# Kernel optimization log

Hardware: AMD Instinct MI355X
Metric: run time of the kernel (lower is better)

## Reference

```python
import jax, jax.numpy as jnp
import numpy as np

B_IN = 30    # input sphere bandwidth
B_MID = 16   # bandwidth after S2 conv
B_OUT = 10   # bandwidth after SO3 conv
F0, F1 = 100, 100
NUM_CLS = 40
EPS = 1e-5


def _wigner_d(l, betas):
    """Real Wigner-d matrices d^l_{mn}(beta) -> [len(betas), 2l+1, 2l+1] (numpy)."""
    betas = np.asarray(betas, np.float64)
    n = 2 * l + 1
    if l == 0:
        return np.ones((betas.size, 1, 1))
    m = np.arange(-l, l)
    c = np.sqrt(l * (l + 1) - m * (m + 1))      # <m+1|J+|m>
    Jp = np.zeros((n, n)); Jp[np.arange(1, n), np.arange(n - 1)] = c
    K = -(Jp - Jp.T) / 2.0                      # K = -i*Jy, real antisymmetric; d = exp(beta*K)
    w, V = np.linalg.eigh(1j * K)
    ph = np.exp(-1j * np.outer(betas, w))
    return np.einsum('ij,bj,kj->bik', V, ph, V.conj()).real


def _dh(b):
    """Driscoll-Healy beta samples and quadrature weights for bandwidth b."""
    k = np.arange(2 * b)
    beta = np.pi * (2 * k + 1) / (4 * b)
    j = np.arange(b)
    w = (2.0 / b) * np.sin(beta) * (np.sin(np.outer(2 * k + 1, 2 * j + 1) * np.pi / (4 * b)) @ (1.0 / (2 * j + 1)))
    return beta, w


def _project(x, b):
    """Point cloud [B,3,N] -> radial distance image on S2 grid [B,1,2b,2b] (beta, alpha)."""
    nb = 2 * b
    r = jnp.linalg.norm(x, axis=1)                                   # [B,N]
    beta = jnp.arccos(jnp.clip(x[:, 2] / jnp.maximum(r, 1e-8), -1.0, 1.0))
    alpha = jnp.mod(jnp.arctan2(x[:, 1], x[:, 0]), 2.0 * np.pi)
    bi = jnp.clip((beta / np.pi * nb).astype(jnp.int32), 0, nb - 1)
    ai = jnp.clip((alpha / (2.0 * np.pi) * nb).astype(jnp.int32), 0, nb - 1)
    Bb = x.shape[0]
    flat = (jnp.arange(Bb)[:, None] * nb * nb + bi * nb + ai).reshape(-1)
    img = jnp.zeros((Bb * nb * nb,), x.dtype).at[flat].max(r.reshape(-1))
    return img.reshape(Bb, 1, nb, nb)


def _s2_fft(x, b_out):
    """x [B,C,2b,2b] (beta,alpha) -> list over l of fhat^l_m [B,C,2l+1] complex."""
    N = x.shape[-1]
    beta, qw = _dh(N // 2)
    G = jnp.fft.fft(x.astype(jnp.complex64), axis=-1)                # coeff of e^{-im alpha}
    out = []
    for l in range(b_out):
        d0 = _wigner_d(l, beta)[:, :, l]                             # d^l_{m,0}(beta_k)
        wd = jnp.asarray(qw[:, None] * d0 * (2 * np.pi / N), jnp.complex64)
        mi = np.arange(-l, l + 1) % N
        out.append(jnp.einsum('km,bckm->bcm', wd, G[..., mi]))
    return out


def _s2_rft(w, b_out, n_alpha):
    """Dirac kernel on equatorial S2 grid (beta=pi/2) -> list over l of [f_in,f_out,2l+1]."""
    alphas = 2 * np.pi * np.arange(n_alpha) / n_alpha
    wc = w.astype(jnp.complex64) / n_alpha
    out = []
    for l in range(b_out):
        m = np.arange(-l, l + 1)
        basis = _wigner_d(l, [np.pi / 2])[0][:, l][:, None] * np.exp(-1j * np.outer(m, alphas))
        out.append(jnp.einsum('mp,iop->iom', jnp.asarray(basis, jnp.complex64), wc))
    return out


def _so3_fft(x, b_out):
    """x [B,C,2b,2b,2b] (beta,alpha,gamma) -> list over l of [B,C,2l+1,2l+1]."""
    N = x.shape[-1]
    beta, qw = _dh(N // 2)
    G = jnp.fft.fft2(x.astype(jnp.complex64), axes=(-2, -1))
    out = []
    for l in range(b_out):
        d = _wigner_d(l, beta)
        wd = jnp.asarray(qw[:, None, None] * d * (2 * np.pi / N) ** 2, jnp.complex64)
        mi = np.arange(-l, l + 1) % N
        out.append(jnp.einsum('kmn,bckmn->bcmn', wd, G[..., mi[:, None], mi[None, :]]))
    return out


def _so3_rft(w, b_out, n_alpha):
    """Dirac kernel on equatorial SO3 grid (beta=pi/2, gamma=0) -> list of [f_in,f_out,2l+1,2l+1]."""
    alphas = 2 * np.pi * np.arange(n_alpha) / n_alpha
    wc = w.astype(jnp.complex64) / n_alpha
    out = []
    for l in range(b_out):
        m = np.arange(-l, l + 1)
        d = _wigner_d(l, [np.pi / 2])[0]
        basis = d[None] * np.exp(-1j * np.outer(alphas, m))[:, :, None]   # [P,2l+1,2l+1]
        out.append(jnp.einsum('pmn,iop->iomn', jnp.asarray(basis, jnp.complex64), wc))
    return out


def _so3_ifft(Z, b_out):
    """Spectral blocks (list over l of [B,f,2l+1,2l+1]) -> x [B,f,2b,2b,2b] real."""
    N = 2 * b_out
    beta, _ = _dh(b_out)
    Bb, f = Z[0].shape[:2]
    M = jnp.zeros((Bb, f, N, N, N), jnp.complex64)
    for l, Zl in enumerate(Z):
        d = jnp.asarray((2 * l + 1) * _wigner_d(l, beta), jnp.complex64)
        mi = np.arange(-l, l + 1) % N
        M = M.at[:, :, :, mi[:, None], mi[None, :]].add(jnp.einsum('kmn,bfmn->bfkmn', d, Zl))
    return (jnp.fft.ifft2(M, axes=(-2, -1)) * (N * N)).real


def _bn_relu(x, g, b):
    mu = x.mean(axis=(0, 2, 3, 4), keepdims=True)
    var = ((x - mu) ** 2).mean(axis=(0, 2, 3, 4), keepdims=True)
    y = (x - mu) * jax.lax.rsqrt(var + EPS) * g[None, :, None, None, None] + b[None, :, None, None, None]
    return jax.nn.relu(y)


def _so3_integrate(x):
    b = x.shape[-1] // 2
    _, qw = _dh(b)
    return jnp.einsum('bfkag,k->bf', x, jnp.asarray(qw, x.dtype)) * (2 * np.pi / (2 * b)) ** 2


def _forward(x, w_s2, bias_s2, bn1_g, bn1_b, w_so3, bias_so3, bn2_g, bn2_b, lin_w, lin_b):
    img = _project(x, B_IN)                                   # [B,1,60,60]
    X = _s2_fft(img, B_MID)
    Y = _s2_rft(w_s2, B_MID, 2 * B_IN)
    # correlation theorem on S2: Z^l_{mn} = sum_i X^l_{i,m} conj(Y^l_{i,n})
    Z = [jnp.einsum('bim,ion->bomn', Xl, jnp.conj(Yl)) for Xl, Yl in zip(X, Y)]
    h = _so3_ifft(Z, B_MID) + bias_s2[None, :, None, None, None]   # [B,100,32,32,32]
    h = _bn_relu(h, bn1_g, bn1_b)
    X2 = _so3_fft(h, B_OUT)
    Y2 = _so3_rft(w_so3, B_OUT, 2 * B_MID)
    # correlation theorem on SO3: Z^l = X^l @ Y^l^dagger (feature-contracted)
    Z2 = [jnp.einsum('bimk,ionk->bomn', Xl, jnp.conj(Yl)) for Xl, Yl in zip(X2, Y2)]
    h2 = _so3_ifft(Z2, B_OUT) + bias_so3[None, :, None, None, None]  # [B,100,20,20,20]
    h2 = _bn_relu(h2, bn2_g, bn2_b)
    feat = _so3_integrate(h2)                                 # [B,100]
    return feat @ lin_w + lin_b                               # cls_logits [B,40]


def setup_inputs() -> dict:
    key = jax.random.key(0)
    ks = jax.random.split(key, 4)
    B, Np = 8, 1024
    return {
        'x': jax.random.normal(ks[0], (B, 3, Np), jnp.float32),
        'w_s2': jax.random.normal(ks[1], (1, F0, 2 * B_IN), jnp.float32) * 0.1,
        'bias_s2': jnp.zeros((F0,), jnp.float32),
        'bn1_g': jnp.ones((F0,), jnp.float32),
        'bn1_b': jnp.zeros((F0,), jnp.float32),
        'w_so3': jax.random.normal(ks[2], (F0, F1, 2 * B_MID), jnp.float32) * 0.1,
        'bias_so3': jnp.zeros((F1,), jnp.float32),
        'bn2_g': jnp.ones((F1,), jnp.float32),
        'bn2_b': jnp.zeros((F1,), jnp.float32),
        'lin_w': jax.random.normal(ks[3], (F1, NUM_CLS), jnp.float32) * 0.1,
        'lin_b': jnp.zeros((NUM_CLS,), jnp.float32),
    }


def reference(x, w_s2, bias_s2, bn1_g, bn1_b, w_so3, bias_so3, bn2_g, bn2_b, lin_w, lin_b):
    return _forward(x, w_s2, bias_s2, bn1_g, bn1_b, w_so3, bias_so3, bn2_g, bn2_b, lin_w, lin_b)
```

## Files before the change

### kernel.cpp

```cpp
#include <hip/hip_runtime.h>
#include <math.h>

#ifndef M_PI
#define M_PI 3.14159265358979323846
#endif

#define TBL_MAGIC 0x5EED5EEDCAFEF00EULL

__device__ const int c_off2[11] = {0,1,10,35,84,165,286,455,680,969,1330};
__device__ const int c_offH[11] = {0,1,7,22,50,95,161,252,372,525,715};
__device__ const int c_T[17] = {0,1,3,6,10,15,21,28,36,45,55,66,78,91,105,120,136};

__device__ constexpr float CS32[32] = {
  1.0f, 0.98078528f, 0.92387953f, 0.83146961f, 0.70710678f, 0.55557023f, 0.38268343f, 0.19509032f,
  0.0f,-0.19509032f,-0.38268343f,-0.55557023f,-0.70710678f,-0.83146961f,-0.92387953f,-0.98078528f,
 -1.0f,-0.98078528f,-0.92387953f,-0.83146961f,-0.70710678f,-0.55557023f,-0.38268343f,-0.19509032f,
  0.0f, 0.19509032f, 0.38268343f, 0.55557023f, 0.70710678f, 0.83146961f, 0.92387953f, 0.98078528f};
__device__ constexpr float SN32[32] = {
  0.0f, 0.19509032f, 0.38268343f, 0.55557023f, 0.70710678f, 0.83146961f, 0.92387953f, 0.98078528f,
  1.0f, 0.98078528f, 0.92387953f, 0.83146961f, 0.70710678f, 0.55557023f, 0.38268343f, 0.19509032f,
  0.0f,-0.19509032f,-0.38268343f,-0.55557023f,-0.70710678f,-0.83146961f,-0.92387953f,-0.98078528f,
 -1.0f,-0.98078528f,-0.92387953f,-0.83146961f,-0.70710678f,-0.55557023f,-0.38268343f,-0.19509032f};

__device__ __forceinline__ int l_from_sq(int off){ int l=0; while((l+1)*(l+1)<=off) l++; return l; }
__device__ __forceinline__ int l_from_offH(int off){ int l=0; while(c_offH[l+1]<=off) l++; return l; }
__device__ __forceinline__ int l_from_T(int c){ int l=0; while(c_T[l+1]<=c) l++; return l; }

__global__ void k_delta(double* Dd, float* Df, const unsigned long long* __restrict__ tflag){
  if (tflag[0]==TBL_MAGIC) return;
  int l = blockIdx.x; int n = 2*l+1; int n2=n*n;
  __shared__ double A[961], T[961], Tm[961];
  for (int idx=threadIdx.x; idx<n2; idx+=1024){
    int r=idx/n, c=idx-r*n;
    double v=0.0;
    if (r==c+1){ double m=(double)(c-l); v = -0.5*sqrt((double)l*(l+1)-m*(m+1)); }
    else if (c==r+1){ double m=(double)(r-l); v = 0.5*sqrt((double)l*(l+1)-m*(m+1)); }
    A[idx] = v*(M_PI*0.5/128.0);
    T[idx] = (r==c)?1.0:0.0;
  }
  __syncthreads();
  for (int j=14; j>=1; --j){
    for (int idx=threadIdx.x; idx<n2; idx+=1024){
      int r=idx/n, c=idx-r*n; double acc=0.0;
      if (r>0)   acc += A[r*n+(r-1)]*T[(r-1)*n+c];
      if (r<n-1) acc += A[r*n+(r+1)]*T[(r+1)*n+c];
      Tm[idx]=acc;
    }
    __syncthreads();
    for (int idx=threadIdx.x; idx<n2; idx+=1024){
      int r=idx/n, c=idx-r*n;
      T[idx] = ((r==c)?1.0:0.0) + Tm[idx]/(double)j;
    }
    __syncthreads();
  }
  for (int s=0; s<7; ++s){
    for (int idx=threadIdx.x; idx<n2; idx+=1024){
      int r=idx/n, c=idx-r*n; double acc=0.0;
      for (int q=0;q<n;q++) acc += T[r*n+q]*T[q*n+c];
      Tm[idx]=acc;
    }
    __syncthreads();
    for (int idx=threadIdx.x; idx<n2; idx+=1024) T[idx]=Tm[idx];
    __syncthreads();
  }
  for (int idx=threadIdx.x; idx<n2; idx+=1024){ Dd[l*961+idx]=T[idx]; Df[l*961+idx]=(float)T[idx]; }
}

__global__ void k_qw(float* qw30, float* qw16, float* qw10, float2* ph32, float2* ph20, float2* ph60,
                     const unsigned long long* __restrict__ tflag){
  if (tflag[0]==TBL_MAGIC) return;
  int t=threadIdx.x;
  if (t<60){
    double beta=M_PI*(2*t+1)/120.0, s=0.0;
    for (int j=0;j<30;j++) s += sin((double)(2*t+1)*(2*j+1)*M_PI/120.0)/(double)(2*j+1);
    qw30[t]=(float)((2.0/30.0)*sin(beta)*s);
    double a=2.0*M_PI*t/60.0; ph60[t]=make_float2((float)cos(a),(float)sin(a));
  }
  if (t<32){
    double beta=M_PI*(2*t+1)/64.0, s=0.0;
    for (int j=0;j<16;j++) s += sin((double)(2*t+1)*(2*j+1)*M_PI/64.0)/(double)(2*j+1);
    qw16[t]=(float)((2.0/16.0)*sin(beta)*s);
    double a=2.0*M_PI*t/32.0; ph32[t]=make_float2((float)cos(a),(float)sin(a));
  }
  if (t<20){
    double beta=M_PI*(2*t+1)/40.0, s=0.0;
    for (int j=0;j<10;j++) s += sin((double)(2*t+1)*(2*j+1)*M_PI/40.0)/(double)(2*j+1);
    qw10[t]=(float)((2.0/10.0)*sin(beta)*s);
    double a=2.0*M_PI*t/20.0; ph20[t]=make_float2((float)cos(a),(float)sin(a));
  }
}

__global__ void k_tables(const double* Dd, const float* qw30, const float* qw16, const float* qw10,
                         float* wd_s2, float* dif16, float* wd16, float* dif10t,
                         const unsigned long long* __restrict__ tflag){
  if (tflag[0]==TBL_MAGIC) return;
  int bid=blockIdx.x;
  __shared__ double cc[32], ss[32];
  int l,k,mode; double beta;
  if (bid<960){ mode=0; l=bid/60; k=bid%60; beta=M_PI*(2*k+1)/120.0; }
  else if (bid<1472){ mode=1; int q=bid-960; l=q/32; k=q%32; beta=M_PI*(2*k+1)/64.0; }
  else { mode=2; int q=bid-1472; l=q/20; k=q%20; beta=M_PI*(2*k+1)/40.0; }
  int n=2*l+1;
  for (int kk=threadIdx.x; kk<=l; kk+=256){ cc[kk]=cos(kk*beta); ss[kk]=sin(kk*beta); }
  __syncthreads();
  const double* D = Dd + l*961;
  if (mode==0){
    for (int mm=threadIdx.x; mm<n; mm+=256){
      int m=mm-l; int p=((m)%4+4)%4; double s=0.0;
      for (int kk=-l; kk<=l; ++kk){
        int ak = kk<0?-kk:kk;
        double c=cc[ak], sn=(kk<0)?-ss[ak]:ss[ak];
        double f=(p==0)?c:(p==1)?sn:(p==2)?-c:-sn;
        s += D[(kk+l)*n+mm]*D[(kk+l)*n+l]*f;
      }
      wd_s2[(l*60+k)*31+mm] = (float)(s*(double)qw30[k]*(2.0*M_PI/60.0));
    }
  } else if (mode==1){
    for (int idx=threadIdx.x; idx<n*n; idx+=256){
      int mm=idx/n, nn=idx-mm*n; int m=mm-l, nb=nn-l;
      int p=((m-nb)%4+4)%4; double s=0.0;
      for (int kk=-l; kk<=l; ++kk){
        int ak = kk<0?-kk:kk;
        double c=cc[ak], sn=(kk<0)?-ss[ak]:ss[ak];
        double f=(p==0)?c:(p==1)?sn:(p==2)?-c:-sn;
        s += D[(kk+l)*n+mm]*D[(kk+l)*n+nn]*f;
      }
      dif16[(size_t)(l*32+k)*961+idx] = (float)((2*l+1)*s);
      if (l<10) wd16[(size_t)(l*32+k)*361+idx] = (float)(s*(double)qw16[k]*(2.0*M_PI/32.0)*(2.0*M_PI/32.0));
    }
  } else {
    for (int idx=threadIdx.x; idx<n*n; idx+=256){
      int mm=idx/n, nn=idx-mm*n; int m=mm-l, nb=nn-l;
      int p=((m-nb)%4+4)%4; double s=0.0;
      for (int kk=-l; kk<=l; ++kk){
        int ak = kk<0?-kk:kk;
        double c=cc[ak], sn=(kk<0)?-ss[ak]:ss[ak];
        double f=(p==0)?c:(p==1)?sn:(p==2)?-c:-sn;
        s += D[(kk+l)*n+mm]*D[(kk+l)*n+nn]*f;
      }
      if (mm>=l){
        int ms=mm-l, n9=nn-l+9;
        dif10t[((size_t)k*10+l)*190 + ms*19 + n9] = (float)((2*l+1)*s);
      }
    }
  }
}

__global__ void k_prep(unsigned long long* tflag, float* img, double2* part){
  int gid = blockIdx.x*256 + threadIdx.x;
  if (gid==0) tflag[0]=TBL_MAGIC;
  for (int i=gid; i<28800; i+=8192) img[i]=0.f;
  for (int i=gid; i<800;   i+=8192) part[i]=make_double2(0.0,0.0);
}

__global__ void k_project(const float* x, float* img){
  int tid = blockIdx.x*256+threadIdx.x;
  if (tid>=8192) return;
  int b=tid>>10, n=tid&1023;
  float px=x[(b*3+0)*1024+n], py=x[(b*3+1)*1024+n], pz=x[(b*3+2)*1024+n];
  float r = sqrtf(px*px+py*py+pz*pz);
  float rc = fmaxf(r, 1e-8f);
  float ct = fminf(1.f, fmaxf(-1.f, pz/rc));
  float beta = acosf(ct);
  float alpha = atan2f(py, px);
  const float TWO_PI = 6.283185307179586f;
  alpha = fmodf(alpha, TWO_PI); if (alpha<0.f) alpha += TWO_PI;
  int bi = (int)(beta/3.14159265358979323846f*60.f); bi = min(59, max(0, bi));
  int ai = (int)(alpha/TWO_PI*60.f);                 ai = min(59, max(0, ai));
  atomicMax((int*)&img[(b*60+bi)*60+ai], __float_as_int(r));
}

__global__ __launch_bounds__(256) void k_front(const float* __restrict__ img, const float2* __restrict__ ph60,
                                               const float* __restrict__ wd_s2, float2* __restrict__ X,
                                               const float* __restrict__ w_s2, const float* __restrict__ Df,
                                               float2* __restrict__ YC,
                                               const float* __restrict__ w_so3, const float2* __restrict__ ph32g,
                                               float2* __restrict__ WH2){
  int bid=blockIdx.x; int t=threadIdx.x;
  if (bid<8){
    int b=bid;
    __shared__ float im[3600];
    __shared__ float2 G[960];
    __shared__ float2 ph[60];
    if (t<60) ph[t]=ph60[t];
    for (int i=t;i<3600;i+=256) im[i]=img[b*3600+i];
    __syncthreads();
    for (int i=t;i<960;i+=256){
      int k=i>>4, m=i&15;
      float sr=0.f, si=0.f;
      const float* imk=&im[k*60];
      for (int a=0;a<60;a++){ float v=imk[a]; float2 p=ph[(m*a)%60]; sr+=v*p.x; si-=v*p.y; }
      G[(k<<4)+m]=make_float2(sr,si);
    }
    __syncthreads();
    int off=t;
    int l=0; while((l+1)*(l+1)<=off) l++;
    int mm=off-l*l; int m=mm-l; int am = m<0?-m:m;
    float xr=0.f, xi=0.f;
    for (int k=0;k<60;k++){
      float w=wd_s2[(l*60+k)*31+mm];
      float2 g=G[(k<<4)+am];
      float gi = (m<0)? -g.y : g.y;
      xr += w*g.x; xi += w*gi;
    }
    X[b*256+off]=make_float2(xr,xi);
  } else if (bid<108){
    int f=bid-8;
    __shared__ float wv[60];
    __shared__ float2 W[16];
    for (int p=t;p<60;p+=256) wv[p]=w_s2[f*60+p];
    __syncthreads();
    if (t<16){
      float sr=0.f, si=0.f;
      for (int p=0;p<60;p++){ float2 p2=ph60[(t*p)%60]; sr+=wv[p]*p2.x; si-=wv[p]*p2.y; }
      W[t]=make_float2(sr/60.f, si/60.f);
    }
    __syncthreads();
    {
      int off=t;
      int l=0; while((l+1)*(l+1)<=off) l++;
      int mm=off-l*l; int m=mm-l; int am=m<0?-m:m;
      float dh=Df[l*961 + mm*(2*l+1) + l];
      float2 wm=W[am];
      float wi = (m>=0)? -wm.y : wm.y;
      YC[f*256+off]=make_float2(dh*wm.x, dh*wi);
    }
  } else {
    int tid=(bid-108)*256+t;
    if (tid<10000){
      int i=tid/100, o=tid-i*100;
      float wv2[32];
      for (int p=0;p<32;p++) wv2[p]=w_so3[(i*100+o)*32+p];
      for (int m=0;m<10;m++){
        float sr=0.f, si=0.f;
        for (int p=0;p<32;p++){ float2 p2=ph32g[(m*p)&31]; sr+=wv2[p]*p2.x; si-=wv2[p]*p2.y; }
        WH2[((size_t)m*100+i)*100+o]=make_float2(sr/32.f, si/32.f);
      }
    }
  }
}

__global__ void k_u(const float2* X, const float* dif16, const float2* ph32g, float2* u){
  int bid=blockIdx.x;
  int l, k, ns0, ns1;
  if (bid < 256){ l = bid>>5; k = bid&31; ns0=0; ns1=l+1; }
  else {
    int q=bid-256; l = 8 + (q>>6); int half=(q>>5)&1; k=q&31;
    int mid=(l+2)>>1;
    ns0 = half? mid : 0; ns1 = half? (l+1) : mid;
  }
  int n=2*l+1;
  __shared__ float d[961];
  __shared__ float2 Xs[8][31];
  __shared__ float2 ph[32];
  int t=threadIdx.x;
  if (t<32) ph[t]=ph32g[t];
  for (int i=t;i<n*n;i+=256) d[i]=dif16[(size_t)(l*32+k)*961+i];
  if (t<8*n){ int b=t/n, mm=t-b*n; Xs[b][mm]=X[b*256+l*l+mm]; }
  __syncthreads();
  int b=t>>5, a=t&31;
  float2* up = u + (size_t)(b*32+k)*4488 + a;
  for (int ns=ns0; ns<ns1; ++ns){
    float ar=0.f, ai=0.f;
    int nn = ns + l;
    for (int mm=0; mm<n; ++mm){
      float2 x=Xs[b][mm];
      float2 p=ph[((mm-l)*a)&31];
      float pr=x.x*p.x-x.y*p.y, pi=x.x*p.y+x.y*p.x;
      float dv=d[mm*n+nn];
      ar += dv*pr; ai += dv*pi;
    }
    up[(size_t)(c_T[l]+ns)*33]=make_float2(ar,ai);
  }
}

#define KH_F 8
__global__ __launch_bounds__(512,4) void k_h(const float2* __restrict__ u, const float2* __restrict__ YC,
                                             float* __restrict__ h, double2* __restrict__ part){
  int bid=blockIdx.x;
  int fg = bid % 13; int rem = bid/13; int kp = rem & 15; int b = rem >> 4;
  int k0 = kp*2;
  int f0 = fg*KH_F; int F_act = (f0+KH_F<=100)? KH_F : (100-f0);

  __shared__ alignas(16) float2 u2[2][4488];
  __shared__ float2 ysc[KH_F*136];
  int t=threadIdx.x;

  {
    const float4* gs = (const float4*)(u + (size_t)(b*32+k0)*4488);
    float4* ls = (float4*)&u2[0][0];
    for (int j=t; j<4488; j+=512) ls[j]=gs[j];
  }
  for (int i=t; i<KH_F*136; i+=512){
    int fi=i/136, c=i-fi*136;
    float2 y=make_float2(0.f,0.f);
    if (fi<F_act){
      int l=l_from_T(c); int ns=c-c_T[l];
      y=YC[(size_t)(f0+fi)*256 + l*l+l+ns];
    }
    ysc[i]=y;
  }
  __syncthreads();

  int kk = t>>8, tt = t&255;
  float* vbase = (float*)&u2[kk][0];

  {
    int ns = tt>>4; int sub = tt&15; int ft = sub>>3; int at = sub&7;
    int a0 = at*4;
    const float2* uk = u2[kk];
    float ar[16], ai[16];
    #pragma unroll
    for (int q=0;q<16;q++){ ar[q]=0.f; ai[q]=0.f; }
    for (int l=ns; l<16; ++l){
      int c = c_T[l]+ns;
      float2 y0=ysc[(ft*4+0)*136+c];
      float2 y1=ysc[(ft*4+1)*136+c];
      float2 y2=ysc[(ft*4+2)*136+c];
      float2 y3=ysc[(ft*4+3)*136+c];
      float2 U0=uk[c*33+a0+0];
      float2 U1=uk[c*33+a0+1];
      float2 U2=uk[c*33+a0+2];
      float2 U3=uk[c*33+a0+3];
      #define CM(j,Y,i_,Ui) \
        ar[(j)*4+(i_)] += (Y).x*(Ui).x - (Y).y*(Ui).y; \
        ai[(j)*4+(i_)] += (Y).x*(Ui).y + (Y).y*(Ui).x;
      CM(0,y0,0,U0) CM(0,y0,1,U1) CM(0,y0,2,U2) CM(0,y0,3,U3)
      CM(1,y1,0,U0) CM(1,y1,1,U1) CM(1,y1,2,U2) CM(1,y1,3,U3)
      CM(2,y2,0,U0) CM(2,y2,1,U1) CM(2,y2,2,U2) CM(2,y2,3,U3)
      CM(3,y3,0,U0) CM(3,y3,1,U1) CM(3,y3,2,U2) CM(3,y3,3,U3)
      #undef CM
    }
    __syncthreads();
    float* vr = vbase;
    float* vi = vbase + 4352;
    #pragma unroll
    for (int j=0;j<4;j++){
      #pragma unroll
      for (int i=0;i<4;i++){
        int fi=ft*4+j, a=a0+i;
        vr[(fi*32+a)*17+ns]=ar[j*4+i];
        vi[(fi*32+a)*17+ns]=ai[j*4+i];
      }
    }
  }
  __syncthreads();

  {
    const float* vr = vbase;
    const float* vi = vbase + 4352;
    int fi=tt>>5, a=tt&31;
    float xr[16], xi[16];
    #pragma unroll
    for (int ns=0;ns<16;ns++){ xr[ns]=vr[(fi*32+a)*17+ns]; xi[ns]=vi[(fi*32+a)*17+ns]; }
    float vr0 = xr[0];
    bool wr = (fi<F_act);
    float* hp = h + ((size_t)(b*100+f0+fi)*32 + (k0+kk))*1024 + a;
    float sf=0.f, qf=0.f;
    #define EMIT(gidx, hv) { float hv_=(hv); if(wr) hp[(gidx)*32]=hv_; sf+=hv_; qf+=hv_*hv_; }
    {
      float se=0.f, so=0.f;
      #pragma unroll
      for (int ns=0; ns<16; ++ns){ if (ns&1) so+=xr[ns]; else se+=xr[ns]; }
      EMIT(0,  2.f*(se+so)-vr0);
      EMIT(16, 2.f*(se-so)-vr0);
    }
    {
      float se=0.f, so=0.f;
      #pragma unroll
      for (int ns=0; ns<16; ++ns){
        const int idx=(ns*8)&31;
        float term = xr[ns]*CS32[idx] - xi[ns]*SN32[idx];
        if (ns&1) so+=term; else se+=term;
      }
      EMIT(8,  2.f*(se+so)-vr0);
      EMIT(24, 2.f*(se-so)-vr0);
    }
    #pragma unroll
    for (int g=1; g<8; ++g){
      float SAe=0.f, SBe=0.f, SAo=0.f, SBo=0.f;
      #pragma unroll
      for (int ns=0; ns<16; ++ns){
        const int idx=(ns*g)&31;
        float A = xr[ns]*CS32[idx];
        float B = xi[ns]*SN32[idx];
        if (ns&1){ SAo+=A; SBo+=B; } else { SAe+=A; SBe+=B; }
      }
      float se1=SAe-SBe, so1=SAo-SBo;
      float se2=SAe+SBe, so2=-(SAo+SBo);
      EMIT(g,      2.f*(se1+so1)-vr0);
      EMIT(g+16,   2.f*(se1-so1)-vr0);
      EMIT(16-g,   2.f*(se2+so2)-vr0);
      EMIT(32-g,   2.f*(se2-so2)-vr0);
    }
    #undef EMIT
    for (int d=16; d>0; d>>=1){ sf += __shfl_down(sf, d, 32); qf += __shfl_down(qf, d, 32); }
    if (a==0 && fi<F_act){
      atomicAdd(&part[b*100+f0+fi].x, (double)sf);
      atomicAdd(&part[b*100+f0+fi].y, (double)qf);
    }
  }
}

__global__ void k_bn2(const double2* __restrict__ partial, int per, const float* g, const float* bb,
                      float* scale, float* shift){
  int f=blockIdx.x*64+threadIdx.x;
  if (f>=100) return;
  double s=0.0, q=0.0;
  for (int b=0;b<8;b++){ double2 v=partial[b*100+f]; s+=v.x; q+=v.y; }
  double cnt=8.0*(double)per;
  double mu=s/cnt, var=q/cnt-mu*mu;
  double sc=(double)g[f]/sqrt(var+1e-5);
  scale[f]=(float)sc; shift[f]=(float)((double)bb[f]-mu*sc);
}

template<int M0>
__device__ __forceinline__ void alpha_dft(const float* __restrict__ yk, float2* __restrict__ tdst, int g){
  float ax0=0.f,ay0=0.f, ax1=0.f,ay1=0.f, ax2=0.f,ay2=0.f, ax3=0.f,ay3=0.f, ax4=0.f,ay4=0.f;
  #pragma unroll
  for (int a=0;a<16;a++){
    float ya=yk[a], yb=yk[a+16];
    float yp=ya+yb, ym=ya-yb;
    #define AM(mi, AX, AY) { \
      const int m_ = M0+mi; \
      const int idx_ = (m_*a)&31; \
      float v_ = (m_&1)? ym : yp; \
      AX += v_*CS32[idx_]; \
      AY -= v_*SN32[idx_]; }
    AM(0,ax0,ay0) AM(1,ax1,ay1) AM(2,ax2,ay2) AM(3,ax3,ay3) AM(4,ax4,ay4)
    #undef AM
  }
  tdst[(M0+0)*33+g]=make_float2(ax0,ay0);
  tdst[(M0+1)*33+g]=make_float2(ax1,ay1);
  tdst[(M0+2)*33+g]=make_float2(ax2,ay2);
  tdst[(M0+3)*33+g]=make_float2(ax3,ay3);
  tdst[(M0+4)*33+g]=make_float2(ax4,ay4);
}

__global__ __launch_bounds__(256) void k_g(const float* __restrict__ h, const float* __restrict__ scale,
                                           const float* __restrict__ shift, const float2* __restrict__ ph32g,
                                           float2* __restrict__ G){
  int bid=blockIdx.x; int kq=bid&7; int bc=bid>>3; int c=bc%100;
  int k0 = kq*4;
  __shared__ float y[4][32*33];
  __shared__ float2 tsc[4][10*33];
  int t=threadIdx.x;
  float sc=scale[c], sh=shift[c];
  {
    const float4* h4 = (const float4*)(h + (size_t)bc*32768 + (size_t)k0*1024);
    for (int i=t;i<1024;i+=256){
      float4 v=h4[i];
      int base=i<<2;
      int kk=base>>10, idx=base&1023, g=idx>>5, a=idx&31;
      float* yw=&y[kk][g*33+a];
      yw[0]=fmaxf(v.x*sc+sh, 0.f);
      yw[1]=fmaxf(v.y*sc+sh, 0.f);
      yw[2]=fmaxf(v.z*sc+sh, 0.f);
      yw[3]=fmaxf(v.w*sc+sh, 0.f);
    }
  }
  __syncthreads();
  int wid=t>>6, lane=t&63;
  {
    int mh=wid&1, kh=wid>>1;
    int kk=kh*2+(lane>>5), g=lane&31;
    const float* yk=&y[kk][g*33];
    if (mh==0) alpha_dft<0>(yk, tsc[kk], g);
    else       alpha_dft<5>(yk, tsc[kk], g);
  }
  __syncthreads();
  if (lane<50){
    int kk=wid;
    int mrow=lane/5, p=lane%5;
    int sa=2*p+1, sb=(p==4)? 0 : 2*p+2;
    const float2* tk=&tsc[kk][mrow*33];
    float2 stA=ph32g[sa];
    float2 stB=ph32g[sb];
    float Aa=0.f,Ba=0.f,Ca=0.f,Da=0.f, Ab=0.f,Bb=0.f,Cb=0.f,Db=0.f;
    #pragma unroll
    for (int half=0; half<2; ++half){
      int ea=(sa*half)&3, eb=(sb*half)&3;
      float2 qa=make_float2(ea==0?1.f:(ea==2?-1.f:0.f), ea==1?1.f:(ea==3?-1.f:0.f));
      float2 qb=make_float2(eb==0?1.f:(eb==2?-1.f:0.f), eb==1?1.f:(eb==3?-1.f:0.f));
      #pragma unroll
      for (int g8=0; g8<8; ++g8){
        int g=half*8+g8;
        float2 ta=tk[g], tb=tk[g+16];
        float tpx=ta.x+tb.x, tpy=ta.y+tb.y;
        float tmx=ta.x-tb.x, tmy=ta.y-tb.y;
        Aa += tmx*qa.x; Ba += tmy*qa.y; Ca += tmy*qa.x; Da += tmx*qa.y;
        Ab += tpx*qb.x; Bb += tpy*qb.y; Cb += tpy*qb.x; Db += tpx*qb.y;
        float nax=qa.x*stA.x - qa.y*stA.y, nay=qa.x*stA.y + qa.y*stA.x; qa=make_float2(nax,nay);
        float nbx=qb.x*stB.x - qb.y*stB.y, nby=qb.x*stB.y + qb.y*stB.x; qb=make_float2(nbx,nby);
      }
    }
    float2* Gp = G + (size_t)(bc*32 + k0+kk)*190 + mrow*19;
    Gp[9+sa]=make_float2(Aa+Ba, Ca-Da);
    Gp[9-sa]=make_float2(Aa-Ba, Ca+Da);
    Gp[9+sb]=make_float2(Ab+Bb, Cb-Db);
    Gp[9-sb]=make_float2(Ab-Bb, Cb+Db);
  }
}

__global__ void k_x2(const float2* __restrict__ G, const float* __restrict__ wd16, float2* __restrict__ X2){
  int tid=blockIdx.x*256+threadIdx.x;
  if (tid>=800*715) return;
  int bc=tid/715, i=tid-bc*715;
  int l=l_from_offH(i); int rem=i-c_offH[l]; int n=2*l+1;
  int m=rem/n, kk2=rem-m*n; int ng=kk2-l;
  int j = m*19+(ng+9);
  const float2* Gp = G + (size_t)bc*32*190 + j;
  const float*  wp = wd16 + (size_t)l*32*361 + (m+l)*n + kk2;
  float ar=0.f, ai=0.f;
  #pragma unroll 8
  for (int k=0;k<32;k++){
    float2 gv=Gp[(size_t)k*190];
    float  wv=wp[(size_t)k*361];
    ar += wv*gv.x; ai += wv*gv.y;
  }
  X2[tid]=make_float2(ar, ai);
}

__global__ void k_A(const float2* __restrict__ X2, const float* __restrict__ Df, float2* __restrict__ A){
  int tid = blockIdx.x*256 + threadIdx.x;
  if (tid >= 800*715) return;
  int bi = tid/715, off = tid - bi*715;
  int l = l_from_offH(off); int rem = off - c_offH[l]; int n = 2*l+1;
  int m = rem/n, nn = rem - m*n;
  const float2* Xp = X2 + (size_t)bi*715 + c_offH[l] + m*n;
  const float* Dp = Df + l*961 + nn*n;
  float ar=0.f, ai=0.f;
  float br=0.f, bis=0.f;
  int kk=0;
  for (; kk+1<n; kk+=2){
    float2 x0 = Xp[kk];   float d0 = Dp[kk];
    float2 x1 = Xp[kk+1]; float d1 = Dp[kk+1];
    ar += x0.x*d0; ai += x0.y*d0;
    br += x1.x*d1; bis += x1.y*d1;
  }
  if (kk<n){ float2 x = Xp[kk]; float dv = Dp[kk]; ar += x.x*dv; ai += x.y*dv; }
  A[tid] = make_float2(ar+br, ai+bis);
}

__global__ void k_z2(const float2* A, const float2* WH2, float2* Z2){
  int bid=blockIdx.x; int b=bid&7; int r=bid>>3;
  int l=l_from_sq(r); int nn=r-l*l; int n=2*l+1; int ns=nn-l;
  int nrow=l+1;
  __shared__ float2 As[100*10];
  int t=threadIdx.x;
  for (int idx=t; idx<100*nrow; idx+=256){
    int i=idx/nrow, m=idx-i*nrow;
    As[idx]=A[(size_t)(b*100+i)*715 + c_offH[l] + m*n + nn];
  }
  __syncthreads();
  int mabs = ns<0?-ns:ns;
  const float2* Wp = WH2 + (size_t)mabs*10000;
  float sgn = (ns>=0)? -1.f : 1.f;
  for (int idx=t; idx<100*nrow; idx+=256){
    int o=idx/nrow, m=idx-o*nrow;
    float zr=0.f, zi=0.f;
    #pragma unroll 4
    for (int i=0;i<100;i++){
      float2 a=As[i*nrow+m];
      float2 w=Wp[i*100+o]; float wr=w.x, wi=sgn*w.y;
      zr += a.x*wr - a.y*wi;
      zi += a.x*wi + a.y*wr;
    }
    Z2[(size_t)(b*100+o)*715 + c_offH[l] + m*n + nn]=make_float2(zr,zi);
  }
}

__global__ __launch_bounds__(256) void k_ifft10(const float2* __restrict__ Z2, const float* __restrict__ dif10t,
                                                const float2* __restrict__ ph20g, float* __restrict__ h2,
                                                double2* __restrict__ part){
  int bid=blockIdx.x; int bf=bid/10, kp=bid-10*bf;
  int k0=kp*2;
  __shared__ float2 Zs[715];
  __shared__ float2 M[2][190];
  __shared__ float2 T[2][200];
  __shared__ float2 ph[20];
  __shared__ float rs[256], rq[256];
  int t=threadIdx.x;
  if (t<20) ph[t]=ph20g[t];
  const float2* Zp = Z2 + (size_t)bf*715;
  for (int i=t;i<715;i+=256) Zs[i]=Zp[i];
  __syncthreads();
  {
    int kk = t>>7, tt = t&127;
    int k = k0+kk;
    for (int i=tt;i<190;i+=128){
      int ms=i/19, n9=i-ms*19; int nsg=n9-9;
      int a2=nsg<0?-nsg:nsg; int l0 = ms>a2?ms:a2;
      float mr=0.f, mi=0.f;
      const float* dp = dif10t + (size_t)k*1900 + i;
      for (int l=l0;l<10;l++){
        float dv=dp[l*190];
        float2 z=Zs[c_offH[l] + ms*(2*l+1) + nsg + l];
        mr += dv*z.x; mi += dv*z.y;
      }
      M[kk][i]=make_float2(mr,mi);
    }
  }
  __syncthreads();
  if (t<200){
    int kk=t/100, j=t-100*kk;
    int g=j/5, ms0=(j%5)*2;
    const float2* Mp0=&M[kk][ms0*19];
    const float2* Mp1=Mp0+19;
    float2 stp=ph[g];
    float2 p=ph[(11*g)%20];
    float tr0=0.f,ti0=0.f,tr1=0.f,ti1=0.f;
    #pragma unroll
    for (int n9=0;n9<19;n9++){
      float2 m0=Mp0[n9], m1=Mp1[n9];
      tr0 += m0.x*p.x - m0.y*p.y;
      ti0 += m0.x*p.y + m0.y*p.x;
      tr1 += m1.x*p.x - m1.y*p.y;
      ti1 += m1.x*p.y + m1.y*p.x;
      float nx=p.x*stp.x - p.y*stp.y, ny=p.x*stp.y + p.y*stp.x;
      p=make_float2(nx,ny);
    }
    T[kk][ms0*20+g]=make_float2(tr0,ti0);
    T[kk][(ms0+1)*20+g]=make_float2(tr1,ti1);
  }
  __syncthreads();
  float sf=0.f, qf=0.f;
  if (t<200){
    int kk=t/100, j=t-100*kk;
    int a=j/5, g0=(j%5)*4;
    const float2* Tk=&T[kk][0];
    float acc0=Tk[g0].x, acc1=Tk[g0+1].x, acc2=Tk[g0+2].x, acc3=Tk[g0+3].x;
    float2 stp=ph[a];
    float2 p=stp;
    #pragma unroll
    for (int ms=1; ms<10; ++ms){
      const float2* Tp=&Tk[ms*20+g0];
      float2 t0=Tp[0], t1=Tp[1], t2=Tp[2], t3=Tp[3];
      acc0 += 2.f*(t0.x*p.x - t0.y*p.y);
      acc1 += 2.f*(t1.x*p.x - t1.y*p.y);
      acc2 += 2.f*(t2.x*p.x - t2.y*p.y);
      acc3 += 2.f*(t3.x*p.x - t3.y*p.y);
      float nx=p.x*stp.x - p.y*stp.y, ny=p.x*stp.y + p.y*stp.x;
      p=make_float2(nx,ny);
    }
    float* hp = h2 + (size_t)bf*8000 + (k0+kk)*400 + a*20 + g0;
    *(float4*)hp = make_float4(acc0,acc1,acc2,acc3);
    sf = acc0+acc1+acc2+acc3;
    qf = acc0*acc0+acc1*acc1+acc2*acc2+acc3*acc3;
  }
  rs[t]=sf; rq[t]=qf; __syncthreads();
  for (int w=128;w>0;w>>=1){ if(t<w){rs[t]+=rs[t+w]; rq[t]+=rq[t+w];} __syncthreads(); }
  if (t==0){
    atomicAdd(&part[bf].x, (double)rs[0]);
    atomicAdd(&part[bf].y, (double)rq[0]);
  }
}

__global__ void k_integrate(const float* h2, const float* scale, const float* shift, const float* qw10, float* feat){
  int bf=blockIdx.x; int f=bf%100; int t=threadIdx.x;
  float sc=scale[f], sh=shift[f];
  const float4* p4=(const float4*)(h2+(size_t)bf*8000);
  float s=0.f;
  for (int i4=t;i4<2000;i4+=256){
    float4 v=p4[i4];
    float qw=qw10[i4/100];
    float r0=fmaxf(v.x*sc+sh,0.f);
    float r1=fmaxf(v.y*sc+sh,0.f);
    float r2=fmaxf(v.z*sc+sh,0.f);
    float r3=fmaxf(v.w*sc+sh,0.f);
    s += (r0+r1+r2+r3)*qw;
  }
  __shared__ float r[256];
  r[t]=s; __syncthreads();
  for (int w=128;w>0;w>>=1){ if(t<w) r[t]+=r[t+w]; __syncthreads(); }
  if (t==0){
    float c=(float)((2.0*M_PI/20.0)*(2.0*M_PI/20.0));
    feat[bf]=r[0]*c;
  }
}

__global__ void k_logits(const float* feat, const float* lw, const float* lb, float* out){
  int t=blockIdx.x*64+threadIdx.x;
  if (t>=320) return;
  int b=t/40, c=t-40*b;
  float s=lb[c];
  for (int f=0;f<100;f++) s += feat[b*100+f]*lw[f*40+c];
  out[t]=s;
}

extern "C" void kernel_launch(void* const* d_in, const int* in_sizes, int n_in,
                              void* d_out, int out_size, void* d_ws, size_t ws_size,
                              hipStream_t stream){
  (void)in_sizes; (void)n_in; (void)out_size; (void)ws_size;
  const float* x    = (const float*)d_in[0];
  const float* w_s2 = (const float*)d_in[1];
  const float* bn1g = (const float*)d_in[3];
  const float* bn1b = (const float*)d_in[4];
  const float* w_so3= (const float*)d_in[5];
  const float* bn2g = (const float*)d_in[7];
  const float* bn2b = (const float*)d_in[8];
  const float* linw = (const float*)d_in[9];
  const float* linb = (const float*)d_in[10];
  float* out = (float*)d_out;

  char* base=(char*)d_ws; size_t off=0;
  auto alloc=[&](size_t bytes)->void*{ void* p=base+off; off=(off+bytes+255)&~(size_t)255; return p; };
  double* Dd   = (double*)alloc((size_t)16*961*8);
  float*  Df   = (float*) alloc((size_t)16*961*4);
  float*  qw30 = (float*) alloc(256);
  float*  qw16 = (float*) alloc(256);
  float*  qw10 = (float*) alloc(256);
  float2* ph60 = (float2*)alloc(512);
  float2* ph32 = (float2*)alloc(256);
  float2* ph20 = (float2*)alloc(256);
  float*  wd_s2= (float*) alloc((size_t)16*60*31*4);
  float*  dif16= (float*) alloc((size_t)16*32*961*4);
  float*  wd16 = (float*) alloc((size_t)10*32*361*4);
  float*  dif10t=(float*) alloc((size_t)20*10*190*4);
  float*  img  = (float*) alloc((size_t)8*3600*4);
  float2* X    = (float2*)alloc((size_t)8*256*8);
  float2* YC   = (float2*)alloc((size_t)100*256*8);
  float2* u    = (float2*)alloc((size_t)8*32*4488*8);
  float*  h    = (float*) alloc((size_t)8*100*32768*4);
  float*  sc1  = (float*) alloc(512);
  float*  sh1  = (float*) alloc(512);
  float2* Gbuf = (float2*)alloc((size_t)800*32*190*8);
  float2* X2   = (float2*)alloc((size_t)800*715*8);
  float2* WH2  = (float2*)alloc((size_t)10*100*100*8);
  float2* A    = (float2*)alloc((size_t)800*715*8);
  float2* Z2   = (float2*)alloc((size_t)800*715*8);
  float*  h2   = (float*) alloc((size_t)8*100*8000*4);
  float*  sc2  = (float*) alloc(512);
  float*  sh2  = (float*) alloc(512);
  float*  feat = (float*) alloc(4096);
  double2* part= (double2*)alloc((size_t)800*16);
  unsigned long long* tflag = (unsigned long long*)alloc(256);

  k_delta<<<16, 1024, 0, stream>>>(Dd, Df, tflag);
  k_qw<<<1, 64, 0, stream>>>(qw30, qw16, qw10, ph32, ph20, ph60, tflag);
  k_tables<<<1672, 256, 0, stream>>>(Dd, qw30, qw16, qw10, wd_s2, dif16, wd16, dif10t, tflag);
  k_prep<<<32, 256, 0, stream>>>(tflag, img, part);
  k_project<<<32, 256, 0, stream>>>(x, img);
  k_front<<<148, 256, 0, stream>>>(img, ph60, wd_s2, X, w_s2, Df, YC, w_so3, ph32, WH2);
  k_u<<<768, 256, 0, stream>>>(X, dif16, ph32, u);
  k_h<<<8*16*13, 512, 0, stream>>>(u, YC, h, part);
  k_bn2<<<2, 64, 0, stream>>>(part, 32768, bn1g, bn1b, sc1, sh1);
  hipMemsetAsync(part, 0, (size_t)800*16, stream);
  k_g<<<800*8, 256, 0, stream>>>(h, sc1, sh1, ph32, Gbuf);
  k_x2<<<(800*715+255)/256, 256, 0, stream>>>(Gbuf, wd16, X2);
  k_A<<<(800*715+255)/256, 256, 0, stream>>>(X2, Df, A);
  k_z2<<<800, 256, 0, stream>>>(A, WH2, Z2);
  k_ifft10<<<8000, 256, 0, stream>>>(Z2, dif10t, ph20, h2, part);
  k_bn2<<<2, 64, 0, stream>>>(part, 8000, bn2g, bn2b, sc2, sh2);
  k_integrate<<<800, 256, 0, stream>>>(h2, sc2, sh2, qw10, feat);
  k_logits<<<5, 64, 0, stream>>>(feat, linw, linb, out);
}
```

Baseline: 422.1 us.

## Restructure k_h to read u from global, split DFT across halves; fuse launches

k_h no longer stages two k-slices of u in shared memory. Each 512-thread block now loops over the two k values, reading u straight from global memory, with all threads covering (ns, f, 8 alpha) per k. The alpha DFT is split by frequency between the two 256-thread halves, so more threads share that work. The separate table kernels k_delta and k_qw are merged into one launch, and the hipMemsetAsync is replaced by zeroing the partials inside k_bn2, which cuts launch overhead. In exchange, k_h relies on global/L2 bandwidth instead of LDS reuse and drops its occupancy hint from launch_bounds.

```diff
diff --git a/kernel.cpp b/kernel.cpp
--- a/kernel.cpp
+++ b/kernel.cpp
@@ -26,8 +26,32 @@
 __device__ __forceinline__ int l_from_offH(int off){ int l=0; while(c_offH[l+1]<=off) l++; return l; }
 __device__ __forceinline__ int l_from_T(int c){ int l=0; while(c_T[l+1]<=c) l++; return l; }
 
-__global__ void k_delta(double* Dd, float* Df, const unsigned long long* __restrict__ tflag){
+__global__ void k_dq(double* Dd, float* Df, float* qw30, float* qw16, float* qw10,
+                     float2* ph32, float2* ph20, float2* ph60,
+                     const unsigned long long* __restrict__ tflag){
   if (tflag[0]==TBL_MAGIC) return;
+  if (blockIdx.x==16){
+    int t=threadIdx.x;
+    if (t<60){
+      double beta=M_PI*(2*t+1)/120.0, s=0.0;
+      for (int j=0;j<30;j++) s += sin((double)(2*t+1)*(2*j+1)*M_PI/120.0)/(double)(2*j+1);
+      qw30[t]=(float)((2.0/30.0)*sin(beta)*s);
+      double a=2.0*M_PI*t/60.0; ph60[t]=make_float2((float)cos(a),(float)sin(a));
+    }
+    if (t<32){
+      double beta=M_PI*(2*t+1)/64.0, s=0.0;
+      for (int j=0;j<16;j++) s += sin((double)(2*t+1)*(2*j+1)*M_PI/64.0)/(double)(2*j+1);
+      qw16[t]=(float)((2.0/16.0)*sin(beta)*s);
+      double a=2.0*M_PI*t/32.0; ph32[t]=make_float2((float)cos(a),(float)sin(a));
+    }
+    if (t<20){
+      double beta=M_PI*(2*t+1)/40.0, s=0.0;
+      for (int j=0;j<10;j++) s += sin((double)(2*t+1)*(2*j+1)*M_PI/40.0)/(double)(2*j+1);
+      qw10[t]=(float)((2.0/10.0)*sin(beta)*s);
+      double a=2.0*M_PI*t/20.0; ph20[t]=make_float2((float)cos(a),(float)sin(a));
+    }
+    return;
+  }
   int l = blockIdx.x; int n = 2*l+1; int n2=n*n;
   __shared__ double A[961], T[961], Tm[961];
   for (int idx=threadIdx.x; idx<n2; idx+=1024){
@@ -64,30 +88,6 @@
     __syncthreads();
   }
   for (int idx=threadIdx.x; idx<n2; idx+=1024){ Dd[l*961+idx]=T[idx]; Df[l*961+idx]=(float)T[idx]; }
-}
-
-__global__ void k_qw(float* qw30, float* qw16, float* qw10, float2* ph32, float2* ph20, float2* ph60,
-                     const unsigned long long* __restrict__ tflag){
-  if (tflag[0]==TBL_MAGIC) return;
-  int t=threadIdx.x;
-  if (t<60){
-    double beta=M_PI*(2*t+1)/120.0, s=0.0;
-    for (int j=0;j<30;j++) s += sin((double)(2*t+1)*(2*j+1)*M_PI/120.0)/(double)(2*j+1);
-    qw30[t]=(float)((2.0/30.0)*sin(beta)*s);
-    double a=2.0*M_PI*t/60.0; ph60[t]=make_float2((float)cos(a),(float)sin(a));
-  }
-  if (t<32){
-    double beta=M_PI*(2*t+1)/64.0, s=0.0;
-    for (int j=0;j<16;j++) s += sin((double)(2*t+1)*(2*j+1)*M_PI/64.0)/(double)(2*j+1);
-    qw16[t]=(float)((2.0/16.0)*sin(beta)*s);
-    double a=2.0*M_PI*t/32.0; ph32[t]=make_float2((float)cos(a),(float)sin(a));
-  }
-  if (t<20){
-    double beta=M_PI*(2*t+1)/40.0, s=0.0;
-    for (int j=0;j<10;j++) s += sin((double)(2*t+1)*(2*j+1)*M_PI/40.0)/(double)(2*j+1);
-    qw10[t]=(float)((2.0/10.0)*sin(beta)*s);
-    double a=2.0*M_PI*t/20.0; ph20[t]=make_float2((float)cos(a),(float)sin(a));
-  }
 }
 
 __global__ void k_tables(const double* Dd, const float* qw30, const float* qw16, const float* qw10,
@@ -275,22 +275,17 @@
 }
 
 #define KH_F 8
-__global__ __launch_bounds__(512,4) void k_h(const float2* __restrict__ u, const float2* __restrict__ YC,
-                                             float* __restrict__ h, double2* __restrict__ part){
+__global__ __launch_bounds__(512) void k_h(const float2* __restrict__ u, const float2* __restrict__ YC,
+                                           float* __restrict__ h, double2* __restrict__ part){
   int bid=blockIdx.x;
   int fg = bid % 13; int rem = bid/13; int kp = rem & 15; int b = rem >> 4;
   int k0 = kp*2;
   int f0 = fg*KH_F; int F_act = (f0+KH_F<=100)? KH_F : (100-f0);
 
-  __shared__ alignas(16) float2 u2[2][4488];
   __shared__ float2 ysc[KH_F*136];
+  __shared__ float vr[4352], vi[4352];
   int t=threadIdx.x;
 
-  {
-    const float4* gs = (const float4*)(u + (size_t)(b*32+k0)*4488);
-    float4* ls = (float4*)&u2[0][0];
-    for (int j=t; j<4488; j+=512) ls[j]=gs[j];
-  }
   for (int i=t; i<KH_F*136; i+=512){
     int fi=i/136, c=i-fi*136;
     float2 y=make_float2(0.f,0.f);
@@ -302,112 +297,113 @@
   }
   __syncthreads();
 
-  int kk = t>>8, tt = t&255;
-  float* vbase = (float*)&u2[kk][0];
-
-  {
-    int ns = tt>>4; int sub = tt&15; int ft = sub>>3; int at = sub&7;
-    int a0 = at*4;
-    const float2* uk = u2[kk];
-    float ar[16], ai[16];
+  int nsB = t>>5, sub=t&31, fB=sub>>2, atB=sub&3, a0=atB*8;
+  int tt=t&255, fi=tt>>5, a=tt&31, half=t>>8;
+  float sf=0.f, qf=0.f;
+
+  for (int kk=0; kk<2; ++kk){
+    const float2* uk = u + (size_t)(b*32+k0+kk)*4488;
+    float ar[8], ai[8];
     #pragma unroll
-    for (int q=0;q<16;q++){ ar[q]=0.f; ai[q]=0.f; }
-    for (int l=ns; l<16; ++l){
-      int c = c_T[l]+ns;
-      float2 y0=ysc[(ft*4+0)*136+c];
-      float2 y1=ysc[(ft*4+1)*136+c];
-      float2 y2=ysc[(ft*4+2)*136+c];
-      float2 y3=ysc[(ft*4+3)*136+c];
-      float2 U0=uk[c*33+a0+0];
-      float2 U1=uk[c*33+a0+1];
-      float2 U2=uk[c*33+a0+2];
-      float2 U3=uk[c*33+a0+3];
-      #define CM(j,Y,i_,Ui) \
-        ar[(j)*4+(i_)] += (Y).x*(Ui).x - (Y).y*(Ui).y; \
-        ai[(j)*4+(i_)] += (Y).x*(Ui).y + (Y).y*(Ui).x;
-      CM(0,y0,0,U0) CM(0,y0,1,U1) CM(0,y0,2,U2) CM(0,y0,3,U3)
-      CM(1,y1,0,U0) CM(1,y1,1,U1) CM(1,y1,2,U2) CM(1,y1,3,U3)
-      CM(2,y2,0,U0) CM(2,y2,1,U1) CM(2,y2,2,U2) CM(2,y2,3,U3)
-      CM(3,y3,0,U0) CM(3,y3,1,U1) CM(3,y3,2,U2) CM(3,y3,3,U3)
-      #undef CM
-    }
-    __syncthreads();
-    float* vr = vbase;
-    float* vi = vbase + 4352;
+    for (int q=0;q<8;q++){ ar[q]=0.f; ai[q]=0.f; }
+    for (int l=nsB; l<16; ++l){
+      int c = c_T[l]+nsB;
+      float2 y = ysc[fB*136+c];
+      const float2* up = &uk[c*33+a0];
+      #pragma unroll
+      for (int i=0;i<8;i++){
+        float2 U = up[i];
+        ar[i] += y.x*U.x - y.y*U.y;
+        ai[i] += y.x*U.y + y.y*U.x;
+      }
+    }
+    if (kk==1) __syncthreads();
     #pragma unroll
-    for (int j=0;j<4;j++){
+    for (int i=0;i<8;i++){
+      vr[(fB*32+a0+i)*17+nsB]=ar[i];
+      vi[(fB*32+a0+i)*17+nsB]=ai[i];
+    }
+    __syncthreads();
+    {
+      float xr[16], xi[16];
       #pragma unroll
-      for (int i=0;i<4;i++){
-        int fi=ft*4+j, a=a0+i;
-        vr[(fi*32+a)*17+ns]=ar[j*4+i];
-        vi[(fi*32+a)*17+ns]=ai[j*4+i];
-      }
-    }
-  }
-  __syncthreads();
-
-  {
-    const float* vr = vbase;
-    const float* vi = vbase + 4352;
-    int fi=tt>>5, a=tt&31;
-    float xr[16], xi[16];
-    #pragma unroll
-    for (int ns=0;ns<16;ns++){ xr[ns]=vr[(fi*32+a)*17+ns]; xi[ns]=vi[(fi*32+a)*17+ns]; }
-    float vr0 = xr[0];
-    bool wr = (fi<F_act);
-    float* hp = h + ((size_t)(b*100+f0+fi)*32 + (k0+kk))*1024 + a;
-    float sf=0.f, qf=0.f;
-    #define EMIT(gidx, hv) { float hv_=(hv); if(wr) hp[(gidx)*32]=hv_; sf+=hv_; qf+=hv_*hv_; }
-    {
-      float se=0.f, so=0.f;
-      #pragma unroll
-      for (int ns=0; ns<16; ++ns){ if (ns&1) so+=xr[ns]; else se+=xr[ns]; }
-      EMIT(0,  2.f*(se+so)-vr0);
-      EMIT(16, 2.f*(se-so)-vr0);
-    }
-    {
-      float se=0.f, so=0.f;
-      #pragma unroll
-      for (int ns=0; ns<16; ++ns){
-        const int idx=(ns*8)&31;
-        float term = xr[ns]*CS32[idx] - xi[ns]*SN32[idx];
-        if (ns&1) so+=term; else se+=term;
-      }
-      EMIT(8,  2.f*(se+so)-vr0);
-      EMIT(24, 2.f*(se-so)-vr0);
-    }
-    #pragma unroll
-    for (int g=1; g<8; ++g){
-      float SAe=0.f, SBe=0.f, SAo=0.f, SBo=0.f;
-      #pragma unroll
-      for (int ns=0; ns<16; ++ns){
-        const int idx=(ns*g)&31;
-        float A = xr[ns]*CS32[idx];
-        float B = xi[ns]*SN32[idx];
-        if (ns&1){ SAo+=A; SBo+=B; } else { SAe+=A; SBe+=B; }
-      }
-      float se1=SAe-SBe, so1=SAo-SBo;
-      float se2=SAe+SBe, so2=-(SAo+SBo);
-      EMIT(g,      2.f*(se1+so1)-vr0);
-      EMIT(g+16,   2.f*(se1-so1)-vr0);
-      EMIT(16-g,   2.f*(se2+so2)-vr0);
-      EMIT(32-g,   2.f*(se2-so2)-vr0);
-    }
-    #undef EMIT
-    for (int d=16; d>0; d>>=1){ sf += __shfl_down(sf, d, 32); qf += __shfl_down(qf, d, 32); }
-    if (a==0 && fi<F_act){
-      atomicAdd(&part[b*100+f0+fi].x, (double)sf);
-      atomicAdd(&part[b*100+f0+fi].y, (double)qf);
-    }
+      for (int q=0;q<16;q++){ xr[q]=vr[(fi*32+a)*17+q]; xi[q]=vi[(fi*32+a)*17+q]; }
+      float vr0 = xr[0];
+      bool wr = (fi<F_act);
+      float* hp = h + ((size_t)(b*100+f0+fi)*32 + (k0+kk))*1024 + a;
+      #define EMIT(gidx, hv) { float hv_=(hv); if(wr) hp[(gidx)*32]=hv_; sf+=hv_; qf+=hv_*hv_; }
+      if (half==0){
+        {
+          float se=0.f, so=0.f;
+          #pragma unroll
+          for (int q=0; q<16; ++q){ if (q&1) so+=xr[q]; else se+=xr[q]; }
+          EMIT(0,  2.f*(se+so)-vr0);
+          EMIT(16, 2.f*(se-so)-vr0);
+        }
+        {
+          float se=0.f, so=0.f;
+          #pragma unroll
+          for (int q=0; q<16; ++q){
+            const int idx=(q*8)&31;
+            float term = xr[q]*CS32[idx] - xi[q]*SN32[idx];
+            if (q&1) so+=term; else se+=term;
+          }
+          EMIT(8,  2.f*(se+so)-vr0);
+          EMIT(24, 2.f*(se-so)-vr0);
+        }
+        #pragma unroll
+        for (int g=1; g<4; ++g){
+          float SAe=0.f, SBe=0.f, SAo=0.f, SBo=0.f;
+          #pragma unroll
+          for (int q=0; q<16; ++q){
+            const int idx=(q*g)&31;
+            float A = xr[q]*CS32[idx];
+            float B = xi[q]*SN32[idx];
+            if (q&1){ SAo+=A; SBo+=B; } else { SAe+=A; SBe+=B; }
+          }
+          float se1=SAe-SBe, so1=SAo-SBo;
+          float se2=SAe+SBe, so2=-(SAo+SBo);
+          EMIT(g,      2.f*(se1+so1)-vr0);
+          EMIT(g+16,   2.f*(se1-so1)-vr0);
+          EMIT(16-g,   2.f*(se2+so2)-vr0);
+          EMIT(32-g,   2.f*(se2-so2)-vr0);
+        }
+      } else {
+        #pragma unroll
+        for (int g=4; g<8; ++g){
+          float SAe=0.f, SBe=0.f, SAo=0.f, SBo=0.f;
+          #pragma unroll
+          for (int q=0; q<16; ++q){
+            const int idx=(q*g)&31;
+            float A = xr[q]*CS32[idx];
+            float B = xi[q]*SN32[idx];
+            if (q&1){ SAo+=A; SBo+=B; } else { SAe+=A; SBe+=B; }
+          }
+          float se1=SAe-SBe, so1=SAo-SBo;
+          float se2=SAe+SBe, so2=-(SAo+SBo);
+          EMIT(g,      2.f*(se1+so1)-vr0);
+          EMIT(g+16,   2.f*(se1-so1)-vr0);
+          EMIT(16-g,   2.f*(se2+so2)-vr0);
+          EMIT(32-g,   2.f*(se2-so2)-vr0);
+        }
+      }
+      #undef EMIT
+    }
+  }
+  for (int d=16; d>0; d>>=1){ sf += __shfl_down(sf, d, 32); qf += __shfl_down(qf, d, 32); }
+  if (a==0 && fi<F_act){
+    atomicAdd(&part[b*100+f0+fi].x, (double)sf);
+    atomicAdd(&part[b*100+f0+fi].y, (double)qf);
   }
 }
 
 __global__ void k_bn2(const double2* __restrict__ partial, int per, const float* g, const float* bb,
-                      float* scale, float* shift){
+                      float* scale, float* shift, double2* partial_w){
   int f=blockIdx.x*64+threadIdx.x;
   if (f>=100) return;
   double s=0.0, q=0.0;
   for (int b=0;b<8;b++){ double2 v=partial[b*100+f]; s+=v.x; q+=v.y; }
+  for (int b=0;b<8;b++){ partial_w[b*100+f]=make_double2(0.0,0.0); }
   double cnt=8.0*(double)per;
   double mu=s/cnt, var=q/cnt-mu*mu;
   double sc=(double)g[f]/sqrt(var+1e-5);
@@ -736,22 +732,20 @@
   double2* part= (double2*)alloc((size_t)800*16);
   unsigned long long* tflag = (unsigned long long*)alloc(256);
 
-  k_delta<<<16, 1024, 0, stream>>>(Dd, Df, tflag);
-  k_qw<<<1, 64, 0, stream>>>(qw30, qw16, qw10, ph32, ph20, ph60, tflag);
+  k_dq<<<17, 1024, 0, stream>>>(Dd, Df, qw30, qw16, qw10, ph32, ph20, ph60, tflag);
   k_tables<<<1672, 256, 0, stream>>>(Dd, qw30, qw16, qw10, wd_s2, dif16, wd16, dif10t, tflag);
   k_prep<<<32, 256, 0, stream>>>(tflag, img, part);
   k_project<<<32, 256, 0, stream>>>(x, img);
   k_front<<<148, 256, 0, stream>>>(img, ph60, wd_s2, X, w_s2, Df, YC, w_so3, ph32, WH2);
   k_u<<<768, 256, 0, stream>>>(X, dif16, ph32, u);
   k_h<<<8*16*13, 512, 0, stream>>>(u, YC, h, part);
-  k_bn2<<<2, 64, 0, stream>>>(part, 32768, bn1g, bn1b, sc1, sh1);
-  hipMemsetAsync(part, 0, (size_t)800*16, stream);
+  k_bn2<<<2, 64, 0, stream>>>(part, 32768, bn1g, bn1b, sc1, sh1, part);
   k_g<<<800*8, 256, 0, stream>>>(h, sc1, sh1, ph32, Gbuf);
   k_x2<<<(800*715+255)/256, 256, 0, stream>>>(Gbuf, wd16, X2);
   k_A<<<(800*715+255)/256, 256, 0, stream>>>(X2, Df, A);
   k_z2<<<800, 256, 0, stream>>>(A, WH2, Z2);
   k_ifft10<<<8000, 256, 0, stream>>>(Z2, dif10t, ph20, h2, part);
-  k_bn2<<<2, 64, 0, stream>>>(part, 8000, bn2g, bn2b, sc2, sh2);
+  k_bn2<<<2, 64, 0, stream>>>(part, 8000, bn2g, bn2b, sc2, sh2, part);
   k_integrate<<<800, 256, 0, stream>>>(h2, sc2, sh2, qw10, feat);
   k_logits<<<5, 64, 0, stream>>>(feat, linw, linb, out);
 }
```

Result: slower. 432.1 us (+2.4%).
